# Optimization experiments

Measured on AMD Instinct MI355X. Metric: run time of the kernel, lower is better.

## Reference

```python
import jax, jax.numpy as jnp
import numpy as np

NQ = 8          # n_qubits
NC = 4          # n_cycles of the angle encoder
PI = np.float32(np.pi)
LAYER_QUBITS = [[0, 1, 2, 3, 4, 5, 6, 7], [1, 3, 5, 7]]  # active qubits per conv layer
FINAL_QUBITS = [3, 7]                                    # active after last pooling
CX = jnp.array([[1, 0, 0, 0], [0, 1, 0, 0], [0, 0, 0, 1], [0, 0, 1, 0]], jnp.complex64)


def apply1(psi, U, q):
    """Apply 1-qubit gate U ((2,2) shared or (B,2,2) batched) on qubit q. psi: (B,2,...,2)."""
    psi = jnp.moveaxis(psi, 1 + q, -1)
    if U.ndim == 3:
        psi = jnp.einsum('bij,b...j->b...i', U, psi)
    else:
        psi = jnp.einsum('ij,...j->...i', U, psi)
    return jnp.moveaxis(psi, -1, 1 + q)


def apply2(psi, U, q0, q1):
    """Apply 2-qubit gate U (4,4) on (q0,q1); q0 is the more-significant wire."""
    psi = jnp.moveaxis(psi, (1 + q0, 1 + q1), (-2, -1))
    sh = psi.shape
    psi = jnp.einsum('ij,...j->...i', U, psi.reshape(sh[:-2] + (4,)))
    return jnp.moveaxis(psi.reshape(sh), (-2, -1), (1 + q0, 1 + q1))


def rz_mat(t):
    return jnp.array([[jnp.exp(-0.5j * t), 0.0], [0.0, jnp.exp(0.5j * t)]]).astype(jnp.complex64)


def ry_mat(t):
    c, s = jnp.cos(t / 2), jnp.sin(t / 2)
    return jnp.array([[c, -s], [s, c]]).astype(jnp.complex64)


def crx_mat(t):
    c = jnp.cos(t / 2).astype(jnp.complex64)
    s = jnp.sin(t / 2).astype(jnp.complex64)
    M = jnp.eye(4, dtype=jnp.complex64)
    return M.at[2, 2].set(c).at[3, 3].set(c).at[2, 3].set(-1j * s).at[3, 2].set(-1j * s)


def u3_mat(t, p, l):
    c, s = jnp.cos(t / 2), jnp.sin(t / 2)
    return jnp.array([[c + 0j, -jnp.exp(1j * l) * s],
                      [jnp.exp(1j * p) * s, jnp.exp(1j * (p + l)) * c]]).astype(jnp.complex64)


def expz(psi, q):
    """<Z_q> = P(q=0) - P(q=1)."""
    p = psi.real ** 2 + psi.imag ** 2
    p = jnp.moveaxis(p, 1 + q, 1).reshape(p.shape[0], 2, -1).sum(-1)
    return p[:, 0] - p[:, 1]


def encode(x):
    """Angle-encoding circuit (circuit_builder): NC cycles of RY(x) + CNOT ring."""
    B = x.shape[0]
    psi = jnp.zeros((B, 2 ** NQ), jnp.complex64).at[:, 0].set(1.0).reshape((B,) + (2,) * NQ)
    for c in range(NC):
        ang = x[:, c * NQ:(c + 1) * NQ]
        cc, ss = jnp.cos(ang / 2), jnp.sin(ang / 2)
        for q in range(NQ):
            U = jnp.stack([jnp.stack([cc[:, q], -ss[:, q]], -1),
                           jnp.stack([ss[:, q], cc[:, q]], -1)], -2).astype(jnp.complex64)
            psi = apply1(psi, U, q)
        for q in range(NQ):
            psi = apply2(psi, CX, q, (q + 1) % NQ)
    return psi


def forward(x, rz_p, ry_p, ry2_p, crx_p, u3_p, u3b_p, W1, b1, W2, b2):
    psi0 = encode(x)
    psi1 = psi0  # deepcopy of encoded state for the second feature map
    for layer in range(2):
        aq = LAYER_QUBITS[layer]
        n = len(aq)
        RZp, RYp, RY2p = rz_mat(rz_p[layer]), ry_mat(ry_p[layer]), ry_mat(ry2_p[layer])
        RZm, RZpl = rz_mat(-PI / 2), rz_mat(PI / 2)
        # circuit 1: ZNOTY-style conv blocks, even pairs then odd pairs
        for parity in (0, 1):
            for i in range(parity, n - 1, 2):
                qc, qt = aq[i], aq[i + 1]
                psi0 = apply1(psi0, RZm, qt)
                psi0 = apply2(psi0, CX, qt, qc)
                psi0 = apply1(psi0, RZp, qc)
                psi0 = apply1(psi0, RYp, qt)
                psi0 = apply2(psi0, CX, qc, qt)
                psi0 = apply1(psi0, RY2p, qt)
                psi0 = apply2(psi0, CX, qt, qc)
                psi0 = apply1(psi0, RZpl, qc)
        remain = [aq[i] for i in range(n) if i % 2 == 1]
        U3a = u3_mat(u3_p[layer, 0], u3_p[layer, 1], u3_p[layer, 2])
        for q in remain:
            psi0 = apply1(psi0, U3a, q)
        # circuit 2: CRX conv blocks, even pairs then odd pairs
        CRXp = crx_mat(crx_p[layer])
        for parity in (0, 1):
            for i in range(parity, n - 1, 2):
                psi1 = apply2(psi1, CRXp, aq[i], aq[i + 1])
        U3b = u3_mat(u3b_p[layer, 0], u3b_p[layer, 1], u3b_p[layer, 2])
        for q in remain:
            psi1 = apply1(psi1, U3b, q)
    xv = jnp.stack([expz(psi0, q) for q in FINAL_QUBITS], 1)  # (B,2)
    yv = jnp.stack([expz(psi1, q) for q in FINAL_QUBITS], 1)  # (B,2)
    feat = jnp.concatenate([xv, yv], 1)                       # (B,4)
    h = jnp.tanh(feat @ W1.T + b1)
    return jax.nn.sigmoid(h @ W2.T + b2)


def setup_inputs() -> dict:
    key = jax.random.key(0)
    ks = jax.random.split(key, 12)
    B = 8192
    return {
        'x': jax.random.normal(ks[0], (B, NC * NQ), jnp.float32),
        'rz_p': jax.random.normal(ks[1], (2,), jnp.float32) * 0.5,
        'ry_p': jax.random.normal(ks[2], (2,), jnp.float32) * 0.5,
        'ry2_p': jax.random.normal(ks[3], (2,), jnp.float32) * 0.5,
        'crx_p': jax.random.normal(ks[4], (2,), jnp.float32) * 0.5,
        'u3_p': jax.random.normal(ks[5], (2, 3), jnp.float32) * 0.5,
        'u3b_p': jax.random.normal(ks[6], (2, 3), jnp.float32) * 0.5,
        'W1': jax.random.normal(ks[7], (15, 4), jnp.float32) * 0.4,
        'b1': jax.random.normal(ks[8], (15,), jnp.float32) * 0.1,
        'W2': jax.random.normal(ks[9], (1, 15), jnp.float32) * 0.25,
        'b2': jax.random.normal(ks[10], (1,), jnp.float32) * 0.1,
    }


def reference(x, rz_p, ry_p, ry2_p, crx_p, u3_p, u3b_p, W1, b1, W2, b2):
    return forward(x, rz_p, ry_p, ry2_p, crx_p, u3_p, u3b_p, W1, b1, W2, b2)
```

## Files before the change

### kernel.cpp

```cpp
#include <hip/hip_runtime.h>

#define DEV __device__ __forceinline__


DEV int lpar(int lane, int m) { return __builtin_popcount(lane & m) & 1; }
constexpr int cpar(int v) { return (v ^ (v >> 1) ^ (v >> 2) ^ (v >> 3)) & 1; }

template<int LM, int SM, int LR, int SR>
DEV void ryr(float* p, float gc, float gs, int lane) {
  const float sg0 = lpar(lane, LR) ? gs : -gs;
  const float sg1 = -sg0;
  if constexpr (LM != 0) {
    float t[16];
    #pragma unroll
    for (int s = 0; s < 16; ++s) t[s] = __shfl_xor(p[s ^ SM], LM);
    #pragma unroll
    for (int s = 0; s < 16; ++s)
      p[s] = gc * p[s] + (cpar(s & SR) ? sg1 : sg0) * t[s];
  } else {
    constexpr int LOW = SM & (-SM);
    #pragma unroll
    for (int s = 0; s < 16; ++s) if (!(s & LOW)) {
      const int s1 = s ^ SM;
      float a = p[s], b = p[s1];
      float sg = cpar(s & SR) ? sg1 : sg0;
      p[s]  = gc * a + sg * b;
      p[s1] = gc * b - sg * a;
    }
  }
}

template<int LM, int SM, int LR, int SR>
DEV void u3_g(float* pr, float* pi, const float* u, int lane) {
  const bool hl = lpar(lane, LR);
  const float d0r = hl ? u[6] : u[0], d0i = hl ? u[7] : u[1];
  const float o0r = hl ? u[4] : u[2], o0i = hl ? u[5] : u[3];
  const float d1r = hl ? u[0] : u[6], d1i = hl ? u[1] : u[7];
  const float o1r = hl ? u[2] : u[4], o1i = hl ? u[3] : u[5];
  if constexpr (LM != 0) {
    float tr[16], ti[16];
    #pragma unroll
    for (int s = 0; s < 16; ++s) {
      tr[s] = __shfl_xor(pr[s ^ SM], LM);
      ti[s] = __shfl_xor(pi[s ^ SM], LM);
    }
    #pragma unroll
    for (int s = 0; s < 16; ++s) {
      const bool c1 = cpar(s & SR);
      const float dr = c1 ? d1r : d0r, di = c1 ? d1i : d0i;
      const float orr = c1 ? o1r : o0r, oi = c1 ? o1i : o0i;
      float ar = pr[s], ai = pi[s];
      pr[s] = dr*ar - di*ai + orr*tr[s] - oi*ti[s];
      pi[s] = dr*ai + di*ar + orr*ti[s] + oi*tr[s];
    }
  } else {
    constexpr int LOW = SM & (-SM);
    #pragma unroll
    for (int s = 0; s < 16; ++s) if (!(s & LOW)) {
      const int s1 = s ^ SM;
      const bool c1 = cpar(s & SR);
      const float dAr = c1 ? d1r : d0r, dAi = c1 ? d1i : d0i;
      const float oAr = c1 ? o1r : o0r, oAi = c1 ? o1i : o0i;
      const float dBr = c1 ? d0r : d1r, dBi = c1 ? d0i : d1i;
      const float oBr = c1 ? o0r : o1r, oBi = c1 ? o0i : o1i;
      float ar = pr[s], ai = pi[s], br = pr[s1], bi = pi[s1];
      pr[s]  = dAr*ar - dAi*ai + oAr*br - oAi*bi;
      pi[s]  = dAr*ai + dAi*ar + oAr*bi + oAi*br;
      pr[s1] = dBr*br - dBi*bi + oBr*ar - oBi*ai;
      pi[s1] = dBr*bi + dBi*br + oBr*ai + oBi*ar;
    }
  }
}

template<int LMt, int SMt, int LRc, int SRc>
DEV void crx_g(float* pr, float* pi, float c, float s_, int lane) {
  const bool hl = lpar(lane, LRc);
  const float cc0 = hl ? c : 1.0f, ss0 = hl ? s_ : 0.0f;
  const float cc1 = hl ? 1.0f : c, ss1 = hl ? 0.0f : s_;
  if constexpr (LMt != 0) {
    float tr[16], ti[16];
    #pragma unroll
    for (int s = 0; s < 16; ++s) {
      tr[s] = __shfl_xor(pr[s ^ SMt], LMt);
      ti[s] = __shfl_xor(pi[s ^ SMt], LMt);
    }
    #pragma unroll
    for (int s = 0; s < 16; ++s) {
      const bool c1 = cpar(s & SRc);
      const float cc = c1 ? cc1 : cc0, ss = c1 ? ss1 : ss0;
      float ar = pr[s], ai = pi[s];
      pr[s] = cc * ar + ss * ti[s];
      pi[s] = cc * ai - ss * tr[s];
    }
  } else {
    constexpr int LOW = SMt & (-SMt);
    #pragma unroll
    for (int s = 0; s < 16; ++s) if (!(s & LOW)) {
      const int s1 = s ^ SMt;
      const bool c1 = cpar(s & SRc);
      const float cc = c1 ? cc1 : cc0, ss = c1 ? ss1 : ss0;
      float ar = pr[s], ai = pi[s], br = pr[s1], bi = pi[s1];
      pr[s]  = cc * ar + ss * bi;
      pi[s]  = cc * ai - ss * br;
      pr[s1] = cc * br + ss * ai;
      pi[s1] = cc * bi - ss * ar;
    }
  }
}

#define U4CLASS(Q)                                                            \
  if constexpr (!(((SRc == 0) && (Q & 2)) || ((SRt == 0) && (Q & 1)))) {      \
    const int r1 = R ^ Q, r2 = r1 ^ 2;                                        \
    const float2 wd = w2[r1 * 4 + r1],       wo = w2[r1 * 4 + (r1 ^ 1)];      \
    const float2 vd = w2[r2 * 4 + r1],       vo = w2[r2 * 4 + (r1 ^ 1)];      \
    _Pragma("unroll")                                                         \
    for (int s = 0; s < 16; ++s)                                              \
      if (((cpar(s & SRc) << 1) | cpar(s & SRt)) == Q) {                      \
        float ar = pr[s], ai = pi[s], br = tr[s], bi = ti[s];                 \
        pr[s] = wd.x*ar - wd.y*ai + wo.x*br - wo.y*bi;                        \
        pi[s] = wd.x*ai + wd.y*ar + wo.x*bi + wo.y*br;                        \
        tr[s] = vd.x*ar - vd.y*ai + vo.x*br - vo.y*bi;                        \
        ti[s] = vd.x*ai + vd.y*ar + vo.x*bi + vo.y*br;                        \
      }                                                                       \
  }

template<int LMc, int SMc, int LMt, int SMt, int LRc, int SRc, int LRt, int SRt>
DEV void u4_g(float* pr, float* pi, const float2* w2, int lane) {
  const int R = (lpar(lane, LRc) << 1) | lpar(lane, LRt);
  float tr[16], ti[16];
  #pragma unroll
  for (int s = 0; s < 16; ++s) {
    float vr = pr[s ^ SMt], vi = pi[s ^ SMt];
    if constexpr (LMt != 0) { vr = __shfl_xor(vr, LMt); vi = __shfl_xor(vi, LMt); }
    tr[s] = vr; ti[s] = vi;
  }
  U4CLASS(0) U4CLASS(1) U4CLASS(2) U4CLASS(3)
  #pragma unroll
  for (int s = 0; s < 16; ++s) {
    float br = tr[s ^ SMc], bi = ti[s ^ SMc];
    if constexpr (LMc != 0) { br = __shfl_xor(br, LMc); bi = __shfl_xor(bi, LMc); }
    pr[s] += br; pi[s] += bi;
  }
}

DEV void u3_make(float t, float p, float l, float* u) {
  float c = __cosf(0.5f * t), s = __sinf(0.5f * t);
  float cp = __cosf(p), sp = __sinf(p);
  float cl = __cosf(l), sl = __sinf(l);
  float cpl = __cosf(p + l), spl = __sinf(p + l);
  u[0] = c;        u[1] = 0.0f;
  u[2] = -cl * s;  u[3] = -sl * s;
  u[4] = cp * s;   u[5] = sp * s;
  u[6] = cpl * c;  u[7] = spl * c;
}

DEV void expz_fin(const float* pr, const float* pi, int lane, float& z3, float& z7) {
  float t3 = 0.0f, t7 = 0.0f;
  #pragma unroll
  for (int s = 0; s < 16; ++s) {
    float p = pr[s] * pr[s] + pi[s] * pi[s];
    t7 += p;
    t3 += (s & 1) ? -p : p;
  }
  if (lpar(lane, 10)) { t3 = -t3; t7 = -t7; }
  #pragma unroll
  for (int m = 1; m < 16; m <<= 1) {
    t3 += __shfl_xor(t3, m);
    t7 += __shfl_xor(t7, m);
  }
  z3 = t3; z7 = t7;
}


__global__ __launch_bounds__(256, 2)
void qcnn_kernel(const float* __restrict__ x,
                 const float* __restrict__ rz_p, const float* __restrict__ ry_p,
                 const float* __restrict__ ry2_p, const float* __restrict__ crx_p,
                 const float* __restrict__ u3_p, const float* __restrict__ u3b_p,
                 const float* __restrict__ W1, const float* __restrict__ b1,
                 const float* __restrict__ W2, const float* __restrict__ b2,
                 float* __restrict__ out, int B) {
  __shared__ __align__(8) float cw[64];
  __shared__ float4 encs[256][5];

  const int tid  = threadIdx.x;
  const int lane = tid & 63;
  const int wave = tid >> 6;
  const int grp  = lane >> 4;
  const int sub  = lane & 15;
  const int gb   = lane & 48;
  const int elem = blockIdx.x * 16 + wave * 4 + grp;
  const int elemc = elem < B ? elem : (B - 1);

  if (tid < 32) {
    const int lay = tid >> 4, e = tid & 15, i4 = e >> 2, j4 = e & 3;
    const int base = tid & 48;
    const float c45 = 0.70710678118654752f;
    float rz = rz_p[lay], ry = ry_p[lay], ry2 = ry2_p[lay];
    float mr = (i4 == j4) ? c45 : 0.0f;
    float mi = (i4 == j4) ? ((i4 & 1) ? -c45 : c45) : 0.0f;
    { int t = (i4 & 1) ? (i4 ^ 2) : i4; int src = base | (t << 2) | j4;
      mr = __shfl(mr, src); mi = __shfl(mi, src); }
    { float cz = __cosf(0.5f * rz), sz = __sinf(0.5f * rz);
      float di = (i4 & 2) ? sz : -sz;
      float nr = cz * mr - di * mi, ni = cz * mi + di * mr; mr = nr; mi = ni; }
    { float cy = __cosf(0.5f * ry), sy = __sinf(0.5f * ry);
      int src = base | ((i4 ^ 1) << 2) | j4;
      float orr = __shfl(mr, src), oii = __shfl(mi, src);
      float sg = (i4 & 1) ? sy : -sy;
      mr = cy * mr + sg * orr; mi = cy * mi + sg * oii; }
    { int t = (i4 & 2) ? (i4 ^ 1) : i4; int src = base | (t << 2) | j4;
      mr = __shfl(mr, src); mi = __shfl(mi, src); }
    { float cy = __cosf(0.5f * ry2), sy = __sinf(0.5f * ry2);
      int src = base | ((i4 ^ 1) << 2) | j4;
      float orr = __shfl(mr, src), oii = __shfl(mi, src);
      float sg = (i4 & 1) ? sy : -sy;
      mr = cy * mr + sg * orr; mi = cy * mi + sg * oii; }
    { int t = (i4 & 1) ? (i4 ^ 2) : i4; int src = base | (t << 2) | j4;
      mr = __shfl(mr, src); mi = __shfl(mi, src); }
    { float di = (i4 & 2) ? c45 : -c45;
      float nr = c45 * mr - di * mi, ni = c45 * mi + di * mr; mr = nr; mi = ni; }
    cw[(lay * 16 + e) * 2]     = mr;
    cw[(lay * 16 + e) * 2 + 1] = mi;
  }

  float2 aa = ((const float2*)x)[(size_t)elemc * 16 + sub];
  float ch0 = __cosf(0.5f * aa.x), sh0 = __sinf(0.5f * aa.x);
  float ch1 = __cosf(0.5f * aa.y), sh1 = __sinf(0.5f * aa.y);

  float cq[8], sq[8];
  #pragma unroll
  for (int q = 0; q < 8; ++q) {
    cq[q] = __shfl((q & 1) ? ch1 : ch0, gb | (q >> 1));
    sq[q] = __shfl((q & 1) ? sh1 : sh0, gb | (q >> 1));
  }

  float p[16];
  {
    float g = ((sub & 8) ? sq[0] : cq[0]) * ((sub & 4) ? sq[2] : cq[2]) *
              ((sub & 2) ? sq[4] : cq[4]) * ((sub & 1) ? sq[6] : cq[6]);
    float h13[4] = {cq[1]*cq[3], cq[1]*sq[3], sq[1]*cq[3], sq[1]*sq[3]};
    float h57[4] = {cq[5]*cq[7], cq[5]*sq[7], sq[5]*cq[7], sq[5]*sq[7]};
    #pragma unroll
    for (int i = 0; i < 4; ++i) h13[i] *= g;
    #pragma unroll
    for (int s = 0; s < 16; ++s) p[s] = h13[s >> 2] * h57[s & 3];
  }

  #define ENC(k, LM, SM, LR, SR) {                                  \
    float gc = __shfl(((k) & 1) ? ch1 : ch0, gb | ((k) >> 1));      \
    float gs = __shfl(((k) & 1) ? sh1 : sh0, gb | ((k) >> 1));      \
    ryr<LM, SM, LR, SR>(p, gc, gs, lane); }

  ENC(8,  8,8, 7,15)  ENC(9,  4,8, 8,8)   ENC(10, 4,4, 12,8)  ENC(11, 2,4, 12,12)
  ENC(12, 2,2, 14,12) ENC(13, 1,2, 14,14) ENC(14, 1,1, 15,14) ENC(15, 8,9, 15,15)
  ENC(16, 12,0, 8,15) ENC(17, 0,12, 15,7) ENC(18, 6,0, 3,15)  ENC(19, 0,6, 15,3)
  ENC(20, 3,0, 1,15)  ENC(21, 0,3, 15,1)  ENC(22, 9,8, 0,15)  ENC(23, 4,9, 15,0)
  ENC(24, 12,12, 2,10) ENC(25, 6,12, 7,8) ENC(26, 6,6, 4,7)   ENC(27, 3,6, 11,4)
  ENC(28, 3,3, 10,11)  ENC(29, 9,11, 5,10) ENC(30, 13,1, 5,5) ENC(31, 8,5, 10,5)
  #undef ENC

  #pragma unroll
  for (int k = 0; k < 4; ++k)
    encs[tid][k] = make_float4(p[4*k], p[4*k+1], p[4*k+2], p[4*k+3]);

  __syncthreads();
  const float2* w0 = (const float2*)cw;
  const float2* w1 = ((const float2*)cw) + 16;

  float pi_[16];
  #pragma unroll
  for (int s = 0; s < 16; ++s) pi_[s] = 0.0f;

  u4_g<10,0,  0,10, 8,10, 5,2 >(p, pi_, w0, lane);
  u4_g<5,0,   0,5,  1,5,  10,1>(p, pi_, w0, lane);
  u4_g<10,8,  4,10, 0,10, 5,0 >(p, pi_, w0, lane);
  u4_g<5,4,   2,5,  0,5,  10,0>(p, pi_, w0, lane);
  u4_g<0,10,  5,0,  5,2,  1,5 >(p, pi_, w0, lane);
  u4_g<0,5,   10,8, 10,1, 0,10>(p, pi_, w0, lane);
  u4_g<4,10,  5,4,  5,0,  0,5 >(p, pi_, w0, lane);
  {
    float ua[8]; u3_make(u3_p[0], u3_p[1], u3_p[2], ua);
    u3_g<0,10, 5,2 >(p, pi_, ua, lane);
    u3_g<0,5,  10,1>(p, pi_, ua, lane);
    u3_g<4,10, 5,0 >(p, pi_, ua, lane);
    u3_g<2,5,  10,0>(p, pi_, ua, lane);
  }
  u4_g<0,10,  0,5,  5,2,  10,1>(p, pi_, w1, lane);
  u4_g<4,10,  2,5,  5,0,  10,0>(p, pi_, w1, lane);
  u4_g<0,5,   4,10, 10,1, 5,0 >(p, pi_, w1, lane);
  {
    float ua[8]; u3_make(u3_p[3], u3_p[4], u3_p[5], ua);
    u3_g<0,5,  10,1>(p, pi_, ua, lane);
    u3_g<2,5,  10,0>(p, pi_, ua, lane);
  }

  float f0, f1;
  expz_fin(p, pi_, lane, f0, f1);

  #pragma unroll
  for (int k = 0; k < 4; ++k) {
    float4 v = encs[tid][k];
    p[4*k] = v.x; p[4*k+1] = v.y; p[4*k+2] = v.z; p[4*k+3] = v.w;
    pi_[4*k] = 0.0f; pi_[4*k+1] = 0.0f; pi_[4*k+2] = 0.0f; pi_[4*k+3] = 0.0f;
  }

  {
    float t = crx_p[0];
    float cc = __cosf(0.5f * t), ss = __sinf(0.5f * t);
    crx_g<0,10, 8,10>(p, pi_, cc, ss, lane);
    crx_g<0,5,  1,5 >(p, pi_, cc, ss, lane);
    crx_g<4,10, 0,10>(p, pi_, cc, ss, lane);
    crx_g<2,5,  0,5 >(p, pi_, cc, ss, lane);
    crx_g<5,0,  5,2 >(p, pi_, cc, ss, lane);
    crx_g<10,8, 10,1>(p, pi_, cc, ss, lane);
    crx_g<5,4,  5,0 >(p, pi_, cc, ss, lane);
  }
  {
    float ub[8]; u3_make(u3b_p[0], u3b_p[1], u3b_p[2], ub);
    u3_g<0,10, 5,2 >(p, pi_, ub, lane);
    u3_g<0,5,  10,1>(p, pi_, ub, lane);
    u3_g<4,10, 5,0 >(p, pi_, ub, lane);
    u3_g<2,5,  10,0>(p, pi_, ub, lane);
  }
  {
    float t = crx_p[1];
    float cc = __cosf(0.5f * t), ss = __sinf(0.5f * t);
    crx_g<0,5,  5,2 >(p, pi_, cc, ss, lane);
    crx_g<2,5,  5,0 >(p, pi_, cc, ss, lane);
    crx_g<4,10, 10,1>(p, pi_, cc, ss, lane);
  }
  {
    float ub[8]; u3_make(u3b_p[3], u3b_p[4], u3b_p[5], ub);
    u3_g<0,5,  10,1>(p, pi_, ub, lane);
    u3_g<2,5,  10,0>(p, pi_, ub, lane);
  }

  float f2, f3;
  expz_fin(p, pi_, lane, f2, f3);

  const int j = (sub < 15) ? sub : 0;
  float acc = W1[j * 4 + 0] * f0 + W1[j * 4 + 1] * f1 +
              W1[j * 4 + 2] * f2 + W1[j * 4 + 3] * f3 + b1[j];
  float e2 = __expf(2.0f * acc);
  float th = (e2 - 1.0f) / (e2 + 1.0f);
  float part = (sub < 15) ? th * W2[j] : 0.0f;
  #pragma unroll
  for (int m = 1; m < 16; m <<= 1) part += __shfl_xor(part, m);

  if (sub == 0 && elem < B) {
    float z = part + b2[0];
    out[elem] = 1.0f / (1.0f + __expf(-z));
  }
}

extern "C" void kernel_launch(void* const* d_in, const int* in_sizes, int n_in,
                              void* d_out, int out_size, void* d_ws, size_t ws_size,
                              hipStream_t stream) {
  (void)n_in; (void)out_size; (void)d_ws; (void)ws_size;
  const float* x     = (const float*)d_in[0];
  const float* rz_p  = (const float*)d_in[1];
  const float* ry_p  = (const float*)d_in[2];
  const float* ry2_p = (const float*)d_in[3];
  const float* crx_p = (const float*)d_in[4];
  const float* u3_p  = (const float*)d_in[5];
  const float* u3b_p = (const float*)d_in[6];
  const float* W1    = (const float*)d_in[7];
  const float* b1    = (const float*)d_in[8];
  const float* W2    = (const float*)d_in[9];
  const float* b2    = (const float*)d_in[10];
  float* out = (float*)d_out;

  const int B = in_sizes[0] / 32;
  const int blocks = (B + 15) / 16;
  qcnn_kernel<<<dim3(blocks), dim3(256), 0, stream>>>(
      x, rz_p, ry_p, ry2_p, crx_p, u3_p, u3b_p, W1, b1, W2, b2, out, B);
}
```

Measured before the change: 115.1 us.

## Spread each 256-amplitude state across a full wave with four amplitudes per lane

Redistributes each batch element's 8-qubit statevector from 16 lanes × 16 registers to 64 lanes × 4 registers, remapping gate qubit masks through constexpr lane/slot translators. This cuts per-thread register pressure, so launch bounds go from 2 to 8 blocks per CU. The LDS buffer for the encoded state is dropped in favour of keeping four values in registers. In exchange, more gates become cross-lane shuffles, reductions span 64 lanes, and each block now handles 4 elements instead of 16, so four times as many blocks are launched.

```diff
diff --git a/kernel.cpp b/kernel.cpp
--- a/kernel.cpp
+++ b/kernel.cpp
@@ -5,22 +5,25 @@
 
 DEV int lpar(int lane, int m) { return __builtin_popcount(lane & m) & 1; }
 constexpr int cpar(int v) { return (v ^ (v >> 1) ^ (v >> 2) ^ (v >> 3)) & 1; }
+
+constexpr int TLm(int LM, int SM) { return (LM << 2) | (SM >> 2); }
+constexpr int TSm(int SM) { return SM & 3; }
 
 template<int LM, int SM, int LR, int SR>
 DEV void ryr(float* p, float gc, float gs, int lane) {
   const float sg0 = lpar(lane, LR) ? gs : -gs;
   const float sg1 = -sg0;
   if constexpr (LM != 0) {
-    float t[16];
-    #pragma unroll
-    for (int s = 0; s < 16; ++s) t[s] = __shfl_xor(p[s ^ SM], LM);
-    #pragma unroll
-    for (int s = 0; s < 16; ++s)
+    float t[4];
+    #pragma unroll
+    for (int s = 0; s < 4; ++s) t[s] = __shfl_xor(p[s ^ SM], LM);
+    #pragma unroll
+    for (int s = 0; s < 4; ++s)
       p[s] = gc * p[s] + (cpar(s & SR) ? sg1 : sg0) * t[s];
   } else {
     constexpr int LOW = SM & (-SM);
     #pragma unroll
-    for (int s = 0; s < 16; ++s) if (!(s & LOW)) {
+    for (int s = 0; s < 4; ++s) if (!(s & LOW)) {
       const int s1 = s ^ SM;
       float a = p[s], b = p[s1];
       float sg = cpar(s & SR) ? sg1 : sg0;
@@ -38,14 +41,14 @@
   const float d1r = hl ? u[0] : u[6], d1i = hl ? u[1] : u[7];
   const float o1r = hl ? u[2] : u[4], o1i = hl ? u[3] : u[5];
   if constexpr (LM != 0) {
-    float tr[16], ti[16];
-    #pragma unroll
-    for (int s = 0; s < 16; ++s) {
+    float tr[4], ti[4];
+    #pragma unroll
+    for (int s = 0; s < 4; ++s) {
       tr[s] = __shfl_xor(pr[s ^ SM], LM);
       ti[s] = __shfl_xor(pi[s ^ SM], LM);
     }
     #pragma unroll
-    for (int s = 0; s < 16; ++s) {
+    for (int s = 0; s < 4; ++s) {
       const bool c1 = cpar(s & SR);
       const float dr = c1 ? d1r : d0r, di = c1 ? d1i : d0i;
       const float orr = c1 ? o1r : o0r, oi = c1 ? o1i : o0i;
@@ -56,7 +59,7 @@
   } else {
     constexpr int LOW = SM & (-SM);
     #pragma unroll
-    for (int s = 0; s < 16; ++s) if (!(s & LOW)) {
+    for (int s = 0; s < 4; ++s) if (!(s & LOW)) {
       const int s1 = s ^ SM;
       const bool c1 = cpar(s & SR);
       const float dAr = c1 ? d1r : d0r, dAi = c1 ? d1i : d0i;
@@ -78,14 +81,14 @@
   const float cc0 = hl ? c : 1.0f, ss0 = hl ? s_ : 0.0f;
   const float cc1 = hl ? 1.0f : c, ss1 = hl ? 0.0f : s_;
   if constexpr (LMt != 0) {
-    float tr[16], ti[16];
-    #pragma unroll
-    for (int s = 0; s < 16; ++s) {
+    float tr[4], ti[4];
+    #pragma unroll
+    for (int s = 0; s < 4; ++s) {
       tr[s] = __shfl_xor(pr[s ^ SMt], LMt);
       ti[s] = __shfl_xor(pi[s ^ SMt], LMt);
     }
     #pragma unroll
-    for (int s = 0; s < 16; ++s) {
+    for (int s = 0; s < 4; ++s) {
       const bool c1 = cpar(s & SRc);
       const float cc = c1 ? cc1 : cc0, ss = c1 ? ss1 : ss0;
       float ar = pr[s], ai = pi[s];
@@ -95,7 +98,7 @@
   } else {
     constexpr int LOW = SMt & (-SMt);
     #pragma unroll
-    for (int s = 0; s < 16; ++s) if (!(s & LOW)) {
+    for (int s = 0; s < 4; ++s) if (!(s & LOW)) {
       const int s1 = s ^ SMt;
       const bool c1 = cpar(s & SRc);
       const float cc = c1 ? cc1 : cc0, ss = c1 ? ss1 : ss0;
@@ -114,7 +117,7 @@
     const float2 wd = w2[r1 * 4 + r1],       wo = w2[r1 * 4 + (r1 ^ 1)];      \
     const float2 vd = w2[r2 * 4 + r1],       vo = w2[r2 * 4 + (r1 ^ 1)];      \
     _Pragma("unroll")                                                         \
-    for (int s = 0; s < 16; ++s)                                              \
+    for (int s = 0; s < 4; ++s)                                               \
       if (((cpar(s & SRc) << 1) | cpar(s & SRt)) == Q) {                      \
         float ar = pr[s], ai = pi[s], br = tr[s], bi = ti[s];                 \
         pr[s] = wd.x*ar - wd.y*ai + wo.x*br - wo.y*bi;                        \
@@ -127,20 +130,34 @@
 template<int LMc, int SMc, int LMt, int SMt, int LRc, int SRc, int LRt, int SRt>
 DEV void u4_g(float* pr, float* pi, const float2* w2, int lane) {
   const int R = (lpar(lane, LRc) << 1) | lpar(lane, LRt);
-  float tr[16], ti[16];
-  #pragma unroll
-  for (int s = 0; s < 16; ++s) {
+  float tr[4], ti[4];
+  #pragma unroll
+  for (int s = 0; s < 4; ++s) {
     float vr = pr[s ^ SMt], vi = pi[s ^ SMt];
     if constexpr (LMt != 0) { vr = __shfl_xor(vr, LMt); vi = __shfl_xor(vi, LMt); }
     tr[s] = vr; ti[s] = vi;
   }
   U4CLASS(0) U4CLASS(1) U4CLASS(2) U4CLASS(3)
   #pragma unroll
-  for (int s = 0; s < 16; ++s) {
+  for (int s = 0; s < 4; ++s) {
     float br = tr[s ^ SMc], bi = ti[s ^ SMc];
     if constexpr (LMc != 0) { br = __shfl_xor(br, LMc); bi = __shfl_xor(bi, LMc); }
     pr[s] += br; pi[s] += bi;
   }
+}
+
+template<int LMc,int SMc,int LMt,int SMt,int LRc,int SRc,int LRt,int SRt>
+DEV void u4o(float* pr, float* pi, const float2* w2, int lane) {
+  u4_g<TLm(LMc,SMc),TSm(SMc), TLm(LMt,SMt),TSm(SMt),
+       TLm(LRc,SRc),TSm(SRc), TLm(LRt,SRt),TSm(SRt)>(pr, pi, w2, lane);
+}
+template<int LM,int SM,int LR,int SR>
+DEV void u3o(float* pr, float* pi, const float* u, int lane) {
+  u3_g<TLm(LM,SM),TSm(SM), TLm(LR,SR),TSm(SR)>(pr, pi, u, lane);
+}
+template<int LMt,int SMt,int LRc,int SRc>
+DEV void crxo(float* pr, float* pi, float c, float s_, int lane) {
+  crx_g<TLm(LMt,SMt),TSm(SMt), TLm(LRc,SRc),TSm(SRc)>(pr, pi, c, s_, lane);
 }
 
 DEV void u3_make(float t, float p, float l, float* u) {
@@ -157,14 +174,14 @@
 DEV void expz_fin(const float* pr, const float* pi, int lane, float& z3, float& z7) {
   float t3 = 0.0f, t7 = 0.0f;
   #pragma unroll
-  for (int s = 0; s < 16; ++s) {
+  for (int s = 0; s < 4; ++s) {
     float p = pr[s] * pr[s] + pi[s] * pi[s];
     t7 += p;
     t3 += (s & 1) ? -p : p;
   }
-  if (lpar(lane, 10)) { t3 = -t3; t7 = -t7; }
-  #pragma unroll
-  for (int m = 1; m < 16; m <<= 1) {
+  if (lpar(lane, 40)) { t3 = -t3; t7 = -t7; }
+  #pragma unroll
+  for (int m = 1; m < 64; m <<= 1) {
     t3 += __shfl_xor(t3, m);
     t7 += __shfl_xor(t7, m);
   }
@@ -172,7 +189,7 @@
 }
 
 
-__global__ __launch_bounds__(256, 2)
+__global__ __launch_bounds__(256, 8)
 void qcnn_kernel(const float* __restrict__ x,
                  const float* __restrict__ rz_p, const float* __restrict__ ry_p,
                  const float* __restrict__ ry2_p, const float* __restrict__ crx_p,
@@ -181,15 +198,12 @@
                  const float* __restrict__ W2, const float* __restrict__ b2,
                  float* __restrict__ out, int B) {
   __shared__ __align__(8) float cw[64];
-  __shared__ float4 encs[256][5];
 
   const int tid  = threadIdx.x;
   const int lane = tid & 63;
   const int wave = tid >> 6;
-  const int grp  = lane >> 4;
   const int sub  = lane & 15;
-  const int gb   = lane & 48;
-  const int elem = blockIdx.x * 16 + wave * 4 + grp;
+  const int elem  = blockIdx.x * 4 + wave;
   const int elemc = elem < B ? elem : (B - 1);
 
   if (tid < 32) {
@@ -231,26 +245,25 @@
   float cq[8], sq[8];
   #pragma unroll
   for (int q = 0; q < 8; ++q) {
-    cq[q] = __shfl((q & 1) ? ch1 : ch0, gb | (q >> 1));
-    sq[q] = __shfl((q & 1) ? sh1 : sh0, gb | (q >> 1));
-  }
-
-  float p[16];
-  {
-    float g = ((sub & 8) ? sq[0] : cq[0]) * ((sub & 4) ? sq[2] : cq[2]) *
-              ((sub & 2) ? sq[4] : cq[4]) * ((sub & 1) ? sq[6] : cq[6]);
-    float h13[4] = {cq[1]*cq[3], cq[1]*sq[3], sq[1]*cq[3], sq[1]*sq[3]};
-    float h57[4] = {cq[5]*cq[7], cq[5]*sq[7], sq[5]*cq[7], sq[5]*sq[7]};
-    #pragma unroll
-    for (int i = 0; i < 4; ++i) h13[i] *= g;
-    #pragma unroll
-    for (int s = 0; s < 16; ++s) p[s] = h13[s >> 2] * h57[s & 3];
+    cq[q] = __shfl((q & 1) ? ch1 : ch0, q >> 1);
+    sq[q] = __shfl((q & 1) ? sh1 : sh0, q >> 1);
+  }
+
+  float p[4];
+  {
+    float g = ((lane & 32) ? sq[0] : cq[0]) * ((lane & 16) ? sq[2] : cq[2]) *
+              ((lane & 8)  ? sq[4] : cq[4]) * ((lane & 4)  ? sq[6] : cq[6]) *
+              ((lane & 2)  ? sq[1] : cq[1]) * ((lane & 1)  ? sq[3] : cq[3]);
+    p[0] = g * cq[5] * cq[7];
+    p[1] = g * cq[5] * sq[7];
+    p[2] = g * sq[5] * cq[7];
+    p[3] = g * sq[5] * sq[7];
   }
 
   #define ENC(k, LM, SM, LR, SR) {                                  \
-    float gc = __shfl(((k) & 1) ? ch1 : ch0, gb | ((k) >> 1));      \
-    float gs = __shfl(((k) & 1) ? sh1 : sh0, gb | ((k) >> 1));      \
-    ryr<LM, SM, LR, SR>(p, gc, gs, lane); }
+    float gc = __shfl(((k) & 1) ? ch1 : ch0, (k) >> 1);             \
+    float gs = __shfl(((k) & 1) ? sh1 : sh0, (k) >> 1);             \
+    ryr<TLm(LM,SM), TSm(SM), TLm(LR,SR), TSm(SR)>(p, gc, gs, lane); }
 
   ENC(8,  8,8, 7,15)  ENC(9,  4,8, 8,8)   ENC(10, 4,4, 12,8)  ENC(11, 2,4, 12,12)
   ENC(12, 2,2, 14,12) ENC(13, 1,2, 14,14) ENC(14, 1,1, 15,14) ENC(15, 8,9, 15,15)
@@ -260,95 +273,87 @@
   ENC(28, 3,3, 10,11)  ENC(29, 9,11, 5,10) ENC(30, 13,1, 5,5) ENC(31, 8,5, 10,5)
   #undef ENC
 
-  #pragma unroll
-  for (int k = 0; k < 4; ++k)
-    encs[tid][k] = make_float4(p[4*k], p[4*k+1], p[4*k+2], p[4*k+3]);
+  const float e0 = p[0], e1 = p[1], e2_ = p[2], e3 = p[3];
 
   __syncthreads();
   const float2* w0 = (const float2*)cw;
   const float2* w1 = ((const float2*)cw) + 16;
 
-  float pi_[16];
-  #pragma unroll
-  for (int s = 0; s < 16; ++s) pi_[s] = 0.0f;
-
-  u4_g<10,0,  0,10, 8,10, 5,2 >(p, pi_, w0, lane);
-  u4_g<5,0,   0,5,  1,5,  10,1>(p, pi_, w0, lane);
-  u4_g<10,8,  4,10, 0,10, 5,0 >(p, pi_, w0, lane);
-  u4_g<5,4,   2,5,  0,5,  10,0>(p, pi_, w0, lane);
-  u4_g<0,10,  5,0,  5,2,  1,5 >(p, pi_, w0, lane);
-  u4_g<0,5,   10,8, 10,1, 0,10>(p, pi_, w0, lane);
-  u4_g<4,10,  5,4,  5,0,  0,5 >(p, pi_, w0, lane);
+  float pi_[4] = {0.0f, 0.0f, 0.0f, 0.0f};
+
+  u4o<10,0,  0,10, 8,10, 5,2 >(p, pi_, w0, lane);
+  u4o<5,0,   0,5,  1,5,  10,1>(p, pi_, w0, lane);
+  u4o<10,8,  4,10, 0,10, 5,0 >(p, pi_, w0, lane);
+  u4o<5,4,   2,5,  0,5,  10,0>(p, pi_, w0, lane);
+  u4o<0,10,  5,0,  5,2,  1,5 >(p, pi_, w0, lane);
+  u4o<0,5,   10,8, 10,1, 0,10>(p, pi_, w0, lane);
+  u4o<4,10,  5,4,  5,0,  0,5 >(p, pi_, w0, lane);
   {
     float ua[8]; u3_make(u3_p[0], u3_p[1], u3_p[2], ua);
-    u3_g<0,10, 5,2 >(p, pi_, ua, lane);
-    u3_g<0,5,  10,1>(p, pi_, ua, lane);
-    u3_g<4,10, 5,0 >(p, pi_, ua, lane);
-    u3_g<2,5,  10,0>(p, pi_, ua, lane);
-  }
-  u4_g<0,10,  0,5,  5,2,  10,1>(p, pi_, w1, lane);
-  u4_g<4,10,  2,5,  5,0,  10,0>(p, pi_, w1, lane);
-  u4_g<0,5,   4,10, 10,1, 5,0 >(p, pi_, w1, lane);
+    u3o<0,10, 5,2 >(p, pi_, ua, lane);
+    u3o<0,5,  10,1>(p, pi_, ua, lane);
+    u3o<4,10, 5,0 >(p, pi_, ua, lane);
+    u3o<2,5,  10,0>(p, pi_, ua, lane);
+  }
+  u4o<0,10,  0,5,  5,2,  10,1>(p, pi_, w1, lane);
+  u4o<4,10,  2,5,  5,0,  10,0>(p, pi_, w1, lane);
+  u4o<0,5,   4,10, 10,1, 5,0 >(p, pi_, w1, lane);
   {
     float ua[8]; u3_make(u3_p[3], u3_p[4], u3_p[5], ua);
-    u3_g<0,5,  10,1>(p, pi_, ua, lane);
-    u3_g<2,5,  10,0>(p, pi_, ua, lane);
+    u3o<0,5,  10,1>(p, pi_, ua, lane);
+    u3o<2,5,  10,0>(p, pi_, ua, lane);
   }
 
   float f0, f1;
   expz_fin(p, pi_, lane, f0, f1);
 
-  #pragma unroll
-  for (int k = 0; k < 4; ++k) {
-    float4 v = encs[tid][k];
-    p[4*k] = v.x; p[4*k+1] = v.y; p[4*k+2] = v.z; p[4*k+3] = v.w;
-    pi_[4*k] = 0.0f; pi_[4*k+1] = 0.0f; pi_[4*k+2] = 0.0f; pi_[4*k+3] = 0.0f;
-  }
+  p[0] = e0; p[1] = e1; p[2] = e2_; p[3] = e3;
+  pi_[0] = 0.0f; pi_[1] = 0.0f; pi_[2] = 0.0f; pi_[3] = 0.0f;
 
   {
     float t = crx_p[0];
     float cc = __cosf(0.5f * t), ss = __sinf(0.5f * t);
-    crx_g<0,10, 8,10>(p, pi_, cc, ss, lane);
-    crx_g<0,5,  1,5 >(p, pi_, cc, ss, lane);
-    crx_g<4,10, 0,10>(p, pi_, cc, ss, lane);
-    crx_g<2,5,  0,5 >(p, pi_, cc, ss, lane);
-    crx_g<5,0,  5,2 >(p, pi_, cc, ss, lane);
-    crx_g<10,8, 10,1>(p, pi_, cc, ss, lane);
-    crx_g<5,4,  5,0 >(p, pi_, cc, ss, lane);
+    crxo<0,10, 8,10>(p, pi_, cc, ss, lane);
+    crxo<0,5,  1,5 >(p, pi_, cc, ss, lane);
+    crxo<4,10, 0,10>(p, pi_, cc, ss, lane);
+    crxo<2,5,  0,5 >(p, pi_, cc, ss, lane);
+    crxo<5,0,  5,2 >(p, pi_, cc, ss, lane);
+    crxo<10,8, 10,1>(p, pi_, cc, ss, lane);
+    crxo<5,4,  5,0 >(p, pi_, cc, ss, lane);
   }
   {
     float ub[8]; u3_make(u3b_p[0], u3b_p[1], u3b_p[2], ub);
-    u3_g<0,10, 5,2 >(p, pi_, ub, lane);
-    u3_g<0,5,  10,1>(p, pi_, ub, lane);
-    u3_g<4,10, 5,0 >(p, pi_, ub, lane);
-    u3_g<2,5,  10,0>(p, pi_, ub, lane);
+    u3o<0,10, 5,2 >(p, pi_, ub, lane);
+    u3o<0,5,  10,1>(p, pi_, ub, lane);
+    u3o<4,10, 5,0 >(p, pi_, ub, lane);
+    u3o<2,5,  10,0>(p, pi_, ub, lane);
   }
   {
     float t = crx_p[1];
     float cc = __cosf(0.5f * t), ss = __sinf(0.5f * t);
-    crx_g<0,5,  5,2 >(p, pi_, cc, ss, lane);
-    crx_g<2,5,  5,0 >(p, pi_, cc, ss, lane);
-    crx_g<4,10, 10,1>(p, pi_, cc, ss, lane);
+    crxo<0,5,  5,2 >(p, pi_, cc, ss, lane);
+    crxo<2,5,  5,0 >(p, pi_, cc, ss, lane);
+    crxo<4,10, 10,1>(p, pi_, cc, ss, lane);
   }
   {
     float ub[8]; u3_make(u3b_p[3], u3b_p[4], u3b_p[5], ub);
-    u3_g<0,5,  10,1>(p, pi_, ub, lane);
-    u3_g<2,5,  10,0>(p, pi_, ub, lane);
+    u3o<0,5,  10,1>(p, pi_, ub, lane);
+    u3o<2,5,  10,0>(p, pi_, ub, lane);
   }
 
   float f2, f3;
   expz_fin(p, pi_, lane, f2, f3);
 
-  const int j = (sub < 15) ? sub : 0;
+  const int j = (lane < 15) ? lane : 0;
   float acc = W1[j * 4 + 0] * f0 + W1[j * 4 + 1] * f1 +
               W1[j * 4 + 2] * f2 + W1[j * 4 + 3] * f3 + b1[j];
   float e2 = __expf(2.0f * acc);
   float th = (e2 - 1.0f) / (e2 + 1.0f);
-  float part = (sub < 15) ? th * W2[j] : 0.0f;
-  #pragma unroll
-  for (int m = 1; m < 16; m <<= 1) part += __shfl_xor(part, m);
-
-  if (sub == 0 && elem < B) {
+  float part = (lane < 15) ? th * W2[j] : 0.0f;
+  #pragma unroll
+  for (int m = 1; m < 64; m <<= 1) part += __shfl_xor(part, m);
+
+  if (lane == 0 && elem < B) {
     float z = part + b2[0];
     out[elem] = 1.0f / (1.0f + __expf(-z));
   }
@@ -372,7 +377,7 @@
   float* out = (float*)d_out;
 
   const int B = in_sizes[0] / 32;
-  const int blocks = (B + 15) / 16;
+  const int blocks = (B + 3) / 4;
   qcnn_kernel<<<dim3(blocks), dim3(256), 0, stream>>>(
       x, rz_p, ry_p, ry2_p, crx_p, u3_p, u3b_p, W1, b1, W2, b2, out, B);
 }
```

Measured after the change: 139.9 us. 1.22x slower.

## Fold U3 gates into adjacent two-qubit gate matrices and precompute gate constants

Applied to the files above, without the earlier changes.

Per block, the U3 tensor products of the first branch are pre-multiplied into the following layer-1 4x4 gate, and in the second branch the U3 pair is folded into the first CRX of layer 1. The resulting fused 4x4 matrices sit in shared memory, so each thread applies fewer separate gates to its statevector. Remaining U3 matrices and CRX cos/sin values are also computed once per block instead of per thread. The fused 4x4 applications cost more per gate than the single-qubit U3s they replace, and correctness depends on the gates commuting or ordering exactly as assumed.

```diff
diff --git a/kernel.cpp b/kernel.cpp
--- a/kernel.cpp
+++ b/kernel.cpp
@@ -181,6 +181,9 @@
                  const float* __restrict__ W2, const float* __restrict__ b2,
                  float* __restrict__ out, int B) {
   __shared__ __align__(8) float cw[64];
+  __shared__ __align__(8) float w1f[32];
+  __shared__ __align__(8) float cx2[32];
+  __shared__ float u3a2[8], u3b2[8], crxc[4];
   __shared__ float4 encs[256][5];
 
   const int tid  = threadIdx.x;
@@ -224,6 +227,57 @@
     cw[(lay * 16 + e) * 2 + 1] = mi;
   }
 
+  if (tid < 64) {
+    if (tid < 16) {
+      const int e = tid, i = e >> 2, j = e & 3;
+      float ua[8]; u3_make(u3_p[0], u3_p[1], u3_p[2], ua);
+      float sr = 0.0f, si = 0.0f;
+      #pragma unroll
+      for (int k = 0; k < 4; ++k) {
+        float wr = cw[(16 + i * 4 + k) * 2], wi = cw[(16 + i * 4 + k) * 2 + 1];
+        float ar = ua[((k >> 1) * 2 + (j >> 1)) * 2];
+        float ai = ua[((k >> 1) * 2 + (j >> 1)) * 2 + 1];
+        float br = ua[((k & 1) * 2 + (j & 1)) * 2];
+        float bi = ua[((k & 1) * 2 + (j & 1)) * 2 + 1];
+        float kr = ar * br - ai * bi, ki = ar * bi + ai * br;
+        sr += wr * kr - wi * ki; si += wr * ki + wi * kr;
+      }
+      w1f[e * 2] = sr; w1f[e * 2 + 1] = si;
+    } else if (tid < 32) {
+      const int e = tid - 16, i = e >> 2, j = e & 3;
+      float ub[8]; u3_make(u3b_p[0], u3b_p[1], u3b_p[2], ub);
+      float t1 = crx_p[1];
+      float cc = __cosf(0.5f * t1), ss = __sinf(0.5f * t1);
+      float kr[4], ki[4];
+      #pragma unroll
+      for (int k = 0; k < 4; ++k) {
+        float ar = ub[((k >> 1) * 2 + (j >> 1)) * 2];
+        float ai = ub[((k >> 1) * 2 + (j >> 1)) * 2 + 1];
+        float br = ub[((k & 1) * 2 + (j & 1)) * 2];
+        float bi = ub[((k & 1) * 2 + (j & 1)) * 2 + 1];
+        kr[k] = ar * br - ai * bi; ki[k] = ar * bi + ai * br;
+      }
+      float sr, si;
+      if (i == 0)      { sr = kr[0]; si = ki[0]; }
+      else if (i == 1) { sr = kr[1]; si = ki[1]; }
+      else if (i == 2) { sr = cc * kr[2] + ss * ki[3]; si = cc * ki[2] - ss * kr[3]; }
+      else             { sr = cc * kr[3] + ss * ki[2]; si = cc * ki[3] - ss * kr[2]; }
+      cx2[e * 2] = sr; cx2[e * 2 + 1] = si;
+    } else if (tid == 32) {
+      float ua[8]; u3_make(u3_p[3], u3_p[4], u3_p[5], ua);
+      #pragma unroll
+      for (int k = 0; k < 8; ++k) u3a2[k] = ua[k];
+    } else if (tid == 33) {
+      float ub[8]; u3_make(u3b_p[3], u3b_p[4], u3b_p[5], ub);
+      #pragma unroll
+      for (int k = 0; k < 8; ++k) u3b2[k] = ub[k];
+    } else if (tid == 34) {
+      float t0 = crx_p[0], t1 = crx_p[1];
+      crxc[0] = __cosf(0.5f * t0); crxc[1] = __sinf(0.5f * t0);
+      crxc[2] = __cosf(0.5f * t1); crxc[3] = __sinf(0.5f * t1);
+    }
+  }
+
   float2 aa = ((const float2*)x)[(size_t)elemc * 16 + sub];
   float ch0 = __cosf(0.5f * aa.x), sh0 = __sinf(0.5f * aa.x);
   float ch1 = __cosf(0.5f * aa.y), sh1 = __sinf(0.5f * aa.y);
@@ -265,8 +319,10 @@
     encs[tid][k] = make_float4(p[4*k], p[4*k+1], p[4*k+2], p[4*k+3]);
 
   __syncthreads();
-  const float2* w0 = (const float2*)cw;
-  const float2* w1 = ((const float2*)cw) + 16;
+  const float2* w0  = (const float2*)cw;
+  const float2* w1  = ((const float2*)cw) + 16;
+  const float2* wf  = (const float2*)w1f;
+  const float2* wc2 = (const float2*)cx2;
 
   float pi_[16];
   #pragma unroll
@@ -279,18 +335,13 @@
   u4_g<0,10,  5,0,  5,2,  1,5 >(p, pi_, w0, lane);
   u4_g<0,5,   10,8, 10,1, 0,10>(p, pi_, w0, lane);
   u4_g<4,10,  5,4,  5,0,  0,5 >(p, pi_, w0, lane);
-  {
-    float ua[8]; u3_make(u3_p[0], u3_p[1], u3_p[2], ua);
-    u3_g<0,10, 5,2 >(p, pi_, ua, lane);
-    u3_g<0,5,  10,1>(p, pi_, ua, lane);
-    u3_g<4,10, 5,0 >(p, pi_, ua, lane);
-    u3_g<2,5,  10,0>(p, pi_, ua, lane);
-  }
-  u4_g<0,10,  0,5,  5,2,  10,1>(p, pi_, w1, lane);
-  u4_g<4,10,  2,5,  5,0,  10,0>(p, pi_, w1, lane);
+  u4_g<0,10,  0,5,  5,2,  10,1>(p, pi_, wf, lane);
+  u4_g<4,10,  2,5,  5,0,  10,0>(p, pi_, wf, lane);
   u4_g<0,5,   4,10, 10,1, 5,0 >(p, pi_, w1, lane);
   {
-    float ua[8]; u3_make(u3_p[3], u3_p[4], u3_p[5], ua);
+    float ua[8];
+    #pragma unroll
+    for (int k = 0; k < 8; ++k) ua[k] = u3a2[k];
     u3_g<0,5,  10,1>(p, pi_, ua, lane);
     u3_g<2,5,  10,0>(p, pi_, ua, lane);
   }
@@ -306,8 +357,7 @@
   }
 
   {
-    float t = crx_p[0];
-    float cc = __cosf(0.5f * t), ss = __sinf(0.5f * t);
+    float cc = crxc[0], ss = crxc[1];
     crx_g<0,10, 8,10>(p, pi_, cc, ss, lane);
     crx_g<0,5,  1,5 >(p, pi_, cc, ss, lane);
     crx_g<4,10, 0,10>(p, pi_, cc, ss, lane);
@@ -316,22 +366,16 @@
     crx_g<10,8, 10,1>(p, pi_, cc, ss, lane);
     crx_g<5,4,  5,0 >(p, pi_, cc, ss, lane);
   }
+  u4_g<0,10,  0,5,  5,2,  10,1>(p, pi_, wc2, lane);
+  u4_g<4,10,  2,5,  5,0,  10,0>(p, pi_, wc2, lane);
   {
-    float ub[8]; u3_make(u3b_p[0], u3b_p[1], u3b_p[2], ub);
-    u3_g<0,10, 5,2 >(p, pi_, ub, lane);
-    u3_g<0,5,  10,1>(p, pi_, ub, lane);
-    u3_g<4,10, 5,0 >(p, pi_, ub, lane);
-    u3_g<2,5,  10,0>(p, pi_, ub, lane);
+    float cc = crxc[2], ss = crxc[3];
+    crx_g<4,10, 10,1>(p, pi_, cc, ss, lane);
   }
   {
-    float t = crx_p[1];
-    float cc = __cosf(0.5f * t), ss = __sinf(0.5f * t);
-    crx_g<0,5,  5,2 >(p, pi_, cc, ss, lane);
-    crx_g<2,5,  5,0 >(p, pi_, cc, ss, lane);
-    crx_g<4,10, 10,1>(p, pi_, cc, ss, lane);
-  }
-  {
-    float ub[8]; u3_make(u3b_p[3], u3b_p[4], u3b_p[5], ub);
+    float ub[8];
+    #pragma unroll
+    for (int k = 0; k < 8; ++k) ub[k] = u3b2[k];
     u3_g<0,5,  10,1>(p, pi_, ub, lane);
     u3_g<2,5,  10,0>(p, pi_, ub, lane);
   }
```

Measured after the change: 129.7 us. +12.7%, slower.
